# Kernel optimization log

Hardware: AMD Instinct MI355X
Metric: run time of the kernel (lower is better)

The kernel has to match this reference:

```python
import jax, jax.numpy as jnp
import numpy as np
from jax import lax

# Static problem sizes (see shape_source)
B, C, N = 32, 512, 64
SENTS_PER_VIDEO = 4
TARGETS_PER_SENT = 2
S = B * SENTS_PER_VIDEO          # 128 sentences
M = S * TARGETS_PER_SENT         # 256 target moments
P = N * (N + 1) // 2             # 2080 valid proposals (upper-tri mask2d)
T_TEMP = 0.1
MARGIN = 0.0
NEG_IOU = 0.5
K_TOP = 1                        # pos_topk
WEIGHT = 1.0


def setup_inputs() -> dict:
    key = jax.random.key(0)
    k1, k2, k3, k4 = jax.random.split(key, 4)
    return {
        "video_feats": jax.random.normal(k1, (B, C, N, N), jnp.float32),
        "sents_feats": jax.random.normal(k2, (S, C), jnp.float32),
        "num_sentences": jnp.full((B,), SENTS_PER_VIDEO, jnp.int32),
        "num_targets": jnp.full((S,), TARGETS_PER_SENT, jnp.int32),
        "iou2d": jax.random.uniform(k3, (S, N, N), jnp.float32),
        "iou2ds": jax.random.uniform(k4, (M, N, N), jnp.float32),
        "mask2d": jnp.triu(jnp.ones((N, N), bool)),
        "epoch": 0,  # < start_DNS_epoch -> DNS branch skipped
    }


def _log_cross_entropy(pos_scores, all_scores, neg_mask, t, m):
    # Faithful to LogCrossEntropy.forward
    pos_exp = jnp.exp((pos_scores - m) / t)
    neg_exp_sum = jnp.sum(jnp.exp(all_scores / t) * neg_mask, axis=-1)
    loss = -((pos_scores - m) / t - jnp.log(pos_exp + neg_exp_sum))
    return jnp.mean(loss)


def _l2_normalize(x, axis=-1, eps=1e-12):
    n = jnp.linalg.norm(x, axis=axis, keepdims=True)
    return x / jnp.maximum(n, eps)


def reference(video_feats, sents_feats, num_sentences, num_targets,
              iou2d, iou2ds, mask2d, epoch):
    # Compact valid proposals (P is static: upper-triangular mask2d)
    idx = jnp.nonzero(mask2d.reshape(-1), size=P)[0]              # (P,)
    v = video_feats.reshape(B, C, N * N)[:, :, idx]               # (B,C,P)
    v = jnp.transpose(v, (0, 2, 1))                               # (B,P,C)
    iou2d_f = iou2d.reshape(S, N * N)[:, idx]                     # (S,P)
    iou2ds_f = iou2ds.reshape(M, N * N)[:, idx]                   # (M,P)

    v = _l2_normalize(v)
    sents = _l2_normalize(sents_feats)

    scatter_s2v = jnp.repeat(jnp.arange(B), num_sentences, total_repeat_length=S)
    scatter_m2s = jnp.repeat(jnp.arange(S), num_targets, total_repeat_length=M)
    scatter_m2v = scatter_s2v[scatter_m2s]

    # top-K proposals per target moment by IoU
    topk_idx = lax.top_k(iou2ds_f, K_TOP)[1]                      # (M,K)
    topk_v = jnp.take_along_axis(v[scatter_m2v], topk_idx[:, :, None], axis=1)  # (M,K,C)

    # inter-video loss
    inter_video_pos = jnp.einsum('mkc,mc->mk', topk_v, sents[scatter_m2s])  # (M,K)
    inter_video_all = jnp.einsum('mkc,sc->mks', topk_v, sents)              # (M,K,S)
    inter_video_neg_mask = (~jnp.eye(S, dtype=bool))[scatter_m2s][:, None, :]  # (M,1,S)
    loss_inter_video = _log_cross_entropy(
        inter_video_pos, inter_video_all, inter_video_neg_mask, T_TEMP, MARGIN)

    # inter-query loss
    inter_query_pos = inter_video_pos                              # (M,K)
    inter_query_all = (sents @ v.reshape(B * P, C).T)[:, None, :]  # (S,1,B*P)
    # pos_mask: block-diagonal per video, refined by IoU > neg_iou inside own block
    onehot = jnp.eye(B, dtype=bool)[scatter_s2v]                   # (S,B)
    pos_mask = (onehot[:, :, None] & (iou2d_f > NEG_IOU)[:, None, :]).reshape(S, B * P)
    inter_query_neg_mask = (~pos_mask)[:, None, :]                 # (S,1,B*P)
    loss_inter_query = _log_cross_entropy(
        inter_query_pos, inter_query_all[scatter_m2s],
        inter_query_neg_mask[scatter_m2s], T_TEMP, MARGIN)

    total = (loss_inter_video + loss_inter_query) * WEIGHT
    return total, loss_inter_video, loss_inter_query
```

## Files before the change

### kernel.cpp

```cpp
#include <hip/hip_runtime.h>
#include <cstdint>

#define BB 32
#define CC 512
#define NSQ 4096
#define SS 128
#define MM 256
#define PP 2080
#define JJ (BB*PP)

#define WS_SN     0
#define WS_SNB    262144
#define WS_IDX    393216
#define WS_IV     401536
#define WS_NEGQ   532608

typedef short bf16x8 __attribute__((ext_vector_type(8)));
typedef float f32x4  __attribute__((ext_vector_type(4)));

__device__ __forceinline__ unsigned short f2bf(float x) {
    unsigned int u = __float_as_uint(x);
    unsigned int r = (u + 0x7fffu + ((u >> 16) & 1u)) >> 16;
    return (unsigned short)r;
}

__global__ void k_prep(const float* __restrict__ sents, float* __restrict__ sn,
                       unsigned short* __restrict__ snb,
                       int* __restrict__ idx, float* __restrict__ negq) {
    const int blk = blockIdx.x, t = threadIdx.x;
    if (blk < 128) {
        __shared__ float red[256];
        const float* row = sents + (size_t)blk * CC;
        float x0 = row[t], x1 = row[t + 256];
        red[t] = x0 * x0 + x1 * x1;
        __syncthreads();
        for (int off = 128; off > 0; off >>= 1) {
            if (t < off) red[t] += red[t + off];
            __syncthreads();
        }
        float rn = 1.0f / fmaxf(sqrtf(red[0]), 1e-12f);
        float y0 = x0 * rn, y1 = x1 * rn;
        sn[(size_t)blk * CC + t]        = y0;
        sn[(size_t)blk * CC + t + 256]  = y1;
        snb[(size_t)blk * CC + t]       = f2bf(y0);
        snb[(size_t)blk * CC + t + 256] = f2bf(y1);
    } else if (blk < 144) {
        int i = (blk - 128) * 256 + t;
        int r = i >> 6, c = i & 63;
        if (c >= r) {
            int p = r * 64 - (r * (r - 1)) / 2 + (c - r);
            idx[p] = i;
        }
    } else {
        if (t < 128) negq[t] = 0.0f;
    }
}

__global__ void k_fused(const float* __restrict__ video, const float* __restrict__ sn,
                        const float* __restrict__ iou2ds, const int* __restrict__ idx,
                        float* __restrict__ iv) {
    const int m = blockIdx.x, t = threadIdx.x;
    __shared__ float sv[256];
    __shared__ int   si[256];
    __shared__ float tvs[512];
    __shared__ float red[256];

    {
        float best = -1e30f; int bi = 1 << 30;
        const float* row = iou2ds + (size_t)m * NSQ;
        for (int p = t; p < PP; p += 256) {
            float v = row[idx[p]];
            if (v > best || (v == best && p < bi)) { best = v; bi = p; }
        }
        sv[t] = best; si[t] = bi;
        __syncthreads();
        for (int off = 128; off > 0; off >>= 1) {
            if (t < off) {
                float v2 = sv[t + off]; int i2 = si[t + off];
                if (v2 > sv[t] || (v2 == sv[t] && i2 < si[t])) { sv[t] = v2; si[t] = i2; }
            }
            __syncthreads();
        }
    }
    const int flat = idx[si[0]];
    const int b = m >> 3;

    const float* base = video + (size_t)b * CC * NSQ + flat;
    float x0 = base[(size_t)t * NSQ];
    float x1 = base[(size_t)(t + 256) * NSQ];
    red[t] = x0 * x0 + x1 * x1;
    __syncthreads();
    for (int off = 128; off > 0; off >>= 1) {
        if (t < off) red[t] += red[t + off];
        __syncthreads();
    }
    float rn = 1.0f / fmaxf(sqrtf(red[0]), 1e-12f);
    tvs[t] = x0 * rn;
    tvs[t + 256] = x1 * rn;
    __syncthreads();

    const int s = t & 127, h = t >> 7;
    const float4* a4 = (const float4*)(tvs + h * 256);
    const float4* b4 = (const float4*)(sn + (size_t)s * CC + h * 256);
    float acc = 0.f;
#pragma unroll 8
    for (int c = 0; c < 64; c++) {
        float4 a = a4[c], bb = b4[c];
        acc += a.x * bb.x + a.y * bb.y + a.z * bb.z + a.w * bb.w;
    }
    __syncthreads();
    red[t] = acc;
    __syncthreads();
    if (t < 128) iv[(size_t)m * SS + t] = red[t] + red[t + 128];
}

#define BK 64
#define LDK 72

__global__ __launch_bounds__(256)
void k_big(const float* __restrict__ video, const unsigned short* __restrict__ snb,
           const float* __restrict__ iou2d, const int* __restrict__ idx,
           float* __restrict__ negq) {
    __shared__ unsigned short sA[128 * LDK];
    __shared__ unsigned short vB[128 * LDK];
    __shared__ int   colb[128], colflat[128];
    __shared__ float colrn[128];
    __shared__ float sqpart[256];
    __shared__ float red[128][17];

    const int t    = threadIdx.x;
    const int w    = t >> 6;
    const int lane = t & 63;
    const int q    = lane >> 4;
    const int l15  = lane & 15;
    const int j0   = blockIdx.x * 128;

    if (t < 128) {
        int col = j0 + t;
        int b = col / PP;
        colb[t] = b;
        colflat[t] = idx[col - b * PP];
    }

    const int jj = t & 127;
    const int kh = t >> 7;
    int colL = j0 + jj;
    int bL = colL / PP;
    int flatL = idx[colL - bL * PP];
    const float* vbase = video + (size_t)bL * (CC * NSQ) + flatL;

    f32x4 acc[2][8];
#pragma unroll
    for (int i = 0; i < 2; i++)
#pragma unroll
        for (int j = 0; j < 8; j++) acc[i][j] = (f32x4){0.f, 0.f, 0.f, 0.f};

    float sqa = 0.f;

    for (int k0 = 0; k0 < CC; k0 += BK) {
        __syncthreads();
#pragma unroll
        for (int it = 0; it < 4; it++) {
            int lin = t + it * 256;
            int row = lin >> 3, kc = (lin & 7) * 8;
            bf16x8 v = *(const bf16x8*)(snb + (size_t)row * CC + k0 + kc);
            *(bf16x8*)(sA + row * LDK + kc) = v;
        }
        {
            const float* vp = vbase + (size_t)(k0 + kh * 32) * NSQ;
#pragma unroll
            for (int g = 0; g < 4; g++) {
                unsigned short buf[8];
#pragma unroll
                for (int i = 0; i < 8; i++) {
                    float x = vp[(size_t)(g * 8 + i) * NSQ];
                    sqa += x * x;
                    buf[i] = f2bf(x);
                }
                *(bf16x8*)(vB + jj * LDK + kh * 32 + g * 8) = *(bf16x8*)buf;
            }
        }
        __syncthreads();
#pragma unroll
        for (int ks = 0; ks < BK; ks += 32) {
            bf16x8 a[2], bfr[8];
#pragma unroll
            for (int rt = 0; rt < 2; rt++) {
                int row = w * 32 + rt * 16 + l15;
                a[rt] = *(const bf16x8*)(sA + row * LDK + ks + q * 8);
            }
#pragma unroll
            for (int ct = 0; ct < 8; ct++) {
                int col = ct * 16 + l15;
                bfr[ct] = *(const bf16x8*)(vB + col * LDK + ks + q * 8);
            }
#pragma unroll
            for (int rt = 0; rt < 2; rt++)
#pragma unroll
                for (int ct = 0; ct < 8; ct++)
                    acc[rt][ct] = __builtin_amdgcn_mfma_f32_16x16x32_bf16(
                        a[rt], bfr[ct], acc[rt][ct], 0, 0, 0);
        }
    }

    sqpart[t] = sqa;
    __syncthreads();
    if (t < 128) colrn[t] = 1.0f / fmaxf(sqrtf(sqpart[t] + sqpart[t + 128]), 1e-12f);
    __syncthreads();

#pragma unroll
    for (int rt = 0; rt < 2; rt++) {
#pragma unroll
        for (int r = 0; r < 4; r++) {
            int s = w * 32 + rt * 16 + q * 4 + r;
            float rowsum = 0.f;
#pragma unroll
            for (int ct = 0; ct < 8; ct++) {
                int c = ct * 16 + l15;
                float sc = acc[rt][ct][r] * colrn[c];
                float e = expf(sc * 10.0f);
                if ((s >> 2) == colb[c]) {
                    if (iou2d[(size_t)s * NSQ + colflat[c]] > 0.5f) e = 0.f;
                }
                rowsum += e;
            }
            red[s][l15] = rowsum;
        }
    }
    __syncthreads();
    if (t < 128) {
        float tot = 0.f;
#pragma unroll
        for (int x = 0; x < 16; x++) tot += red[t][x];
        atomicAdd(&negq[t], tot);
    }
}

__global__ void k_final(const float* __restrict__ iv, const float* __restrict__ negq,
                        float* __restrict__ out) {
    const int t = threadIdx.x;
    __shared__ float rv[256], rq[256];
    const float* row = iv + (size_t)t * SS;
    const int ms = t >> 1;
    float pos = row[ms];
    float nv = 0.f;
    for (int s = 0; s < SS; s++) {
        float e = expf(row[s] * 10.0f);
        if (s == ms) e = 0.f;
        nv += e;
    }
    float pe = expf(pos * 10.0f);
    float lv = logf(pe + nv) - pos * 10.0f;
    float lq = logf(pe + negq[ms]) - pos * 10.0f;
    rv[t] = lv; rq[t] = lq;
    __syncthreads();
    for (int off = 128; off > 0; off >>= 1) {
        if (t < off) { rv[t] += rv[t + off]; rq[t] += rq[t + off]; }
        __syncthreads();
    }
    if (t == 0) {
        float liv = rv[0] / 256.f, liq = rq[0] / 256.f;
        out[0] = liv + liq;
        out[1] = liv;
        out[2] = liq;
    }
}

extern "C" void kernel_launch(void* const* d_in, const int* in_sizes, int n_in,
                              void* d_out, int out_size, void* d_ws, size_t ws_size,
                              hipStream_t stream) {
    const float* video  = (const float*)d_in[0];
    const float* sents  = (const float*)d_in[1];
    const float* iou2d  = (const float*)d_in[4];
    const float* iou2ds = (const float*)d_in[5];
    float* out = (float*)d_out;

    char* ws = (char*)d_ws;
    float*          sn   = (float*)(ws + WS_SN);
    unsigned short* snb  = (unsigned short*)(ws + WS_SNB);
    int*            idx  = (int*)(ws + WS_IDX);
    float*          iv   = (float*)(ws + WS_IV);
    float*          negq = (float*)(ws + WS_NEGQ);

    k_prep <<<145, 256, 0, stream>>>(sents, sn, snb, idx, negq);
    k_big  <<<JJ / 128, 256, 0, stream>>>(video, snb, iou2d, idx, negq);
    k_fused<<<MM,  256, 0, stream>>>(video, sn, iou2ds, idx, iv);
    k_final<<<1,   256, 0, stream>>>(iv, negq, out);
}
```

Baseline: 438.2 us.

## Fuse all stages into one persistent cooperative kernel with atomic job queue

Replaces the four separate launches with a single cooperative persistent kernel of 512 blocks. The blocks run the prep stage, sync across the grid, then pull GEMM tiles and top-1 moment jobs from an atomic counter, sync across the grid again, and block 0 computes the final loss. The GEMM path also register-prefetches the next K-slab of video features to overlap global loads with MFMA work. This removes launch gaps and tail effects at the cost of grid syncs, extra register pressure from the 32-float prefetch buffer, and a residency requirement for the cooperative launch, with the old kernels kept as a fallback.

```diff
diff --git a/kernel.cpp b/kernel.cpp
--- a/kernel.cpp
+++ b/kernel.cpp
@@ -1,5 +1,8 @@
 #include <hip/hip_runtime.h>
+#include <hip/hip_cooperative_groups.h>
 #include <cstdint>
+
+namespace cg = cooperative_groups;
 
 #define BB 32
 #define CC 512
@@ -8,12 +11,15 @@
 #define MM 256
 #define PP 2080
 #define JJ (BB*PP)
+#define NTILE (JJ/128)
+#define NJOBS (NTILE + MM)
 
 #define WS_SN     0
 #define WS_SNB    262144
 #define WS_IDX    393216
 #define WS_IV     401536
 #define WS_NEGQ   532608
+#define WS_CTR    533120
 
 typedef short bf16x8 __attribute__((ext_vector_type(8)));
 typedef float f32x4  __attribute__((ext_vector_type(4)));
@@ -22,6 +28,275 @@
     unsigned int u = __float_as_uint(x);
     unsigned int r = (u + 0x7fffu + ((u >> 16) & 1u)) >> 16;
     return (unsigned short)r;
+}
+
+#define BK 64
+#define LDK 72
+
+struct SMemG {
+    unsigned short sA[128 * LDK];
+    unsigned short vB[128 * LDK];
+    int   colb[128];
+    int   colflat[128];
+    float colrn[128];
+    float sqpart[256];
+    float red[128][17];
+};
+struct SMemM {
+    float sv[256];
+    int   si[256];
+    float tvs[512];
+    float red[256];
+};
+struct SMemP {
+    float red[256];
+};
+union SMem { SMemG g; SMemM m; SMemP p; };
+
+__global__ __launch_bounds__(256, 2)
+void k_all(const float* __restrict__ video, const float* __restrict__ sents,
+           const float* __restrict__ iou2d, const float* __restrict__ iou2ds,
+           float* __restrict__ sn, unsigned short* __restrict__ snb,
+           int* __restrict__ idx, float* __restrict__ iv,
+           float* __restrict__ negq, int* __restrict__ ctr,
+           float* __restrict__ out)
+{
+    __shared__ SMem sm;
+    __shared__ int jobS;
+    const int t   = threadIdx.x;
+    const int blk = blockIdx.x;
+    cg::grid_group grid = cg::this_grid();
+
+    if (blk < 128) {
+        const float* row = sents + (size_t)blk * CC;
+        float x0 = row[t], x1 = row[t + 256];
+        sm.p.red[t] = x0 * x0 + x1 * x1;
+        __syncthreads();
+        for (int off = 128; off > 0; off >>= 1) {
+            if (t < off) sm.p.red[t] += sm.p.red[t + off];
+            __syncthreads();
+        }
+        float rn = 1.0f / fmaxf(sqrtf(sm.p.red[0]), 1e-12f);
+        float y0 = x0 * rn, y1 = x1 * rn;
+        sn[(size_t)blk * CC + t]        = y0;
+        sn[(size_t)blk * CC + t + 256]  = y1;
+        snb[(size_t)blk * CC + t]       = f2bf(y0);
+        snb[(size_t)blk * CC + t + 256] = f2bf(y1);
+    } else if (blk < 144) {
+        int i = (blk - 128) * 256 + t;
+        int r = i >> 6, c = i & 63;
+        if (c >= r) {
+            int p = r * 64 - (r * (r - 1)) / 2 + (c - r);
+            idx[p] = i;
+        }
+    } else if (blk == 144) {
+        if (t < 128) negq[t] = 0.0f;
+        if (t == 128) *ctr = 0;
+    }
+    grid.sync();
+
+    const int w    = t >> 6;
+    const int lane = t & 63;
+    const int q    = lane >> 4;
+    const int l15  = lane & 15;
+
+    for (;;) {
+        __syncthreads();
+        if (t == 0) jobS = atomicAdd(ctr, 1);
+        __syncthreads();
+        const int job = jobS;
+        if (job >= NJOBS) break;
+
+        if (job < NTILE) {
+            const int j0 = job * 128;
+            if (t < 128) {
+                int col = j0 + t;
+                int b = col / PP;
+                sm.g.colb[t] = b;
+                sm.g.colflat[t] = idx[col - b * PP];
+            }
+            const int jj = t & 127;
+            const int kh = t >> 7;
+            int colL = j0 + jj;
+            int bL = colL / PP;
+            int flatL = idx[colL - bL * PP];
+            const float* vbase = video + (size_t)bL * (CC * NSQ) + flatL;
+
+            f32x4 acc[2][8];
+#pragma unroll
+            for (int i = 0; i < 2; i++)
+#pragma unroll
+                for (int j = 0; j < 8; j++) acc[i][j] = (f32x4){0.f, 0.f, 0.f, 0.f};
+            float sqa = 0.f;
+
+            float pre[32];
+            {
+                const float* vp = vbase + (size_t)(kh * 32) * NSQ;
+#pragma unroll
+                for (int i = 0; i < 32; i++) pre[i] = vp[(size_t)i * NSQ];
+            }
+
+            for (int k0 = 0; k0 < CC; k0 += BK) {
+                __syncthreads();
+#pragma unroll
+                for (int it = 0; it < 4; it++) {
+                    int lin = t + it * 256;
+                    int row = lin >> 3, kc = (lin & 7) * 8;
+                    bf16x8 v = *(const bf16x8*)(snb + (size_t)row * CC + k0 + kc);
+                    *(bf16x8*)(sm.g.sA + row * LDK + kc) = v;
+                }
+#pragma unroll
+                for (int g = 0; g < 4; g++) {
+                    unsigned short buf[8];
+#pragma unroll
+                    for (int i = 0; i < 8; i++) {
+                        float x = pre[g * 8 + i];
+                        sqa += x * x;
+                        buf[i] = f2bf(x);
+                    }
+                    *(bf16x8*)(sm.g.vB + jj * LDK + kh * 32 + g * 8) = *(bf16x8*)buf;
+                }
+                __syncthreads();
+                if (k0 + BK < CC) {
+                    const float* vp = vbase + (size_t)(k0 + BK + kh * 32) * NSQ;
+#pragma unroll
+                    for (int i = 0; i < 32; i++) pre[i] = vp[(size_t)i * NSQ];
+                }
+#pragma unroll
+                for (int ks = 0; ks < BK; ks += 32) {
+                    bf16x8 a[2], bfr[8];
+#pragma unroll
+                    for (int rt = 0; rt < 2; rt++) {
+                        int row = w * 32 + rt * 16 + l15;
+                        a[rt] = *(const bf16x8*)(sm.g.sA + row * LDK + ks + q * 8);
+                    }
+#pragma unroll
+                    for (int ct = 0; ct < 8; ct++) {
+                        int col = ct * 16 + l15;
+                        bfr[ct] = *(const bf16x8*)(sm.g.vB + col * LDK + ks + q * 8);
+                    }
+#pragma unroll
+                    for (int rt = 0; rt < 2; rt++)
+#pragma unroll
+                        for (int ct = 0; ct < 8; ct++)
+                            acc[rt][ct] = __builtin_amdgcn_mfma_f32_16x16x32_bf16(
+                                a[rt], bfr[ct], acc[rt][ct], 0, 0, 0);
+                }
+            }
+
+            sm.g.sqpart[t] = sqa;
+            __syncthreads();
+            if (t < 128)
+                sm.g.colrn[t] = 1.0f / fmaxf(sqrtf(sm.g.sqpart[t] + sm.g.sqpart[t + 128]), 1e-12f);
+            __syncthreads();
+
+#pragma unroll
+            for (int rt = 0; rt < 2; rt++) {
+#pragma unroll
+                for (int r = 0; r < 4; r++) {
+                    int s = w * 32 + rt * 16 + q * 4 + r;
+                    float rowsum = 0.f;
+#pragma unroll
+                    for (int ct = 0; ct < 8; ct++) {
+                        int c = ct * 16 + l15;
+                        float sc = acc[rt][ct][r] * sm.g.colrn[c];
+                        float e = expf(sc * 10.0f);
+                        if ((s >> 2) == sm.g.colb[c]) {
+                            if (iou2d[(size_t)s * NSQ + sm.g.colflat[c]] > 0.5f) e = 0.f;
+                        }
+                        rowsum += e;
+                    }
+                    sm.g.red[s][l15] = rowsum;
+                }
+            }
+            __syncthreads();
+            if (t < 128) {
+                float tot = 0.f;
+#pragma unroll
+                for (int x = 0; x < 16; x++) tot += sm.g.red[t][x];
+                atomicAdd(&negq[t], tot);
+            }
+        } else {
+            const int m = job - NTILE;
+            {
+                float best = -1e30f; int bi = 1 << 30;
+                const float* row = iou2ds + (size_t)m * NSQ;
+                for (int p = t; p < PP; p += 256) {
+                    float v = row[idx[p]];
+                    if (v > best || (v == best && p < bi)) { best = v; bi = p; }
+                }
+                sm.m.sv[t] = best; sm.m.si[t] = bi;
+                __syncthreads();
+                for (int off = 128; off > 0; off >>= 1) {
+                    if (t < off) {
+                        float v2 = sm.m.sv[t + off]; int i2 = sm.m.si[t + off];
+                        if (v2 > sm.m.sv[t] || (v2 == sm.m.sv[t] && i2 < sm.m.si[t])) {
+                            sm.m.sv[t] = v2; sm.m.si[t] = i2;
+                        }
+                    }
+                    __syncthreads();
+                }
+            }
+            const int flat = idx[sm.m.si[0]];
+            const int b = m >> 3;
+
+            const float* base = video + (size_t)b * CC * NSQ + flat;
+            float x0 = base[(size_t)t * NSQ];
+            float x1 = base[(size_t)(t + 256) * NSQ];
+            sm.m.red[t] = x0 * x0 + x1 * x1;
+            __syncthreads();
+            for (int off = 128; off > 0; off >>= 1) {
+                if (t < off) sm.m.red[t] += sm.m.red[t + off];
+                __syncthreads();
+            }
+            float rn = 1.0f / fmaxf(sqrtf(sm.m.red[0]), 1e-12f);
+            sm.m.tvs[t] = x0 * rn;
+            sm.m.tvs[t + 256] = x1 * rn;
+            __syncthreads();
+
+            const int s = t & 127, h = t >> 7;
+            const float4* a4 = (const float4*)(sm.m.tvs + h * 256);
+            const float4* b4 = (const float4*)(sn + (size_t)s * CC + h * 256);
+            float acc2 = 0.f;
+#pragma unroll 8
+            for (int c = 0; c < 64; c++) {
+                float4 a = a4[c], bb = b4[c];
+                acc2 += a.x * bb.x + a.y * bb.y + a.z * bb.z + a.w * bb.w;
+            }
+            __syncthreads();
+            sm.m.red[t] = acc2;
+            __syncthreads();
+            if (t < 128) iv[(size_t)m * SS + t] = sm.m.red[t] + sm.m.red[t + 128];
+        }
+    }
+    grid.sync();
+
+    if (blk == 0) {
+        const float* row = iv + (size_t)t * SS;
+        const int ms = t >> 1;
+        float pos = row[ms];
+        float nv = 0.f;
+        for (int s2 = 0; s2 < SS; s2++) {
+            float e = expf(row[s2] * 10.0f);
+            if (s2 == ms) e = 0.f;
+            nv += e;
+        }
+        float pe = expf(pos * 10.0f);
+        float lv = logf(pe + nv) - pos * 10.0f;
+        float lq = logf(pe + negq[ms]) - pos * 10.0f;
+        sm.m.sv[t] = lv; sm.m.red[t] = lq;
+        __syncthreads();
+        for (int off = 128; off > 0; off >>= 1) {
+            if (t < off) { sm.m.sv[t] += sm.m.sv[t + off]; sm.m.red[t] += sm.m.red[t + off]; }
+            __syncthreads();
+        }
+        if (t == 0) {
+            float liv = sm.m.sv[0] / 256.f, liq = sm.m.red[0] / 256.f;
+            out[0] = liv + liq;
+            out[1] = liv;
+            out[2] = liq;
+        }
+    }
 }
 
 __global__ void k_prep(const float* __restrict__ sents, float* __restrict__ sn,
@@ -64,7 +339,6 @@
     __shared__ int   si[256];
     __shared__ float tvs[512];
     __shared__ float red[256];
-
     {
         float best = -1e30f; int bi = 1 << 30;
         const float* row = iou2ds + (size_t)m * NSQ;
@@ -84,7 +358,6 @@
     }
     const int flat = idx[si[0]];
     const int b = m >> 3;
-
     const float* base = video + (size_t)b * CC * NSQ + flat;
     float x0 = base[(size_t)t * NSQ];
     float x1 = base[(size_t)(t + 256) * NSQ];
@@ -98,7 +371,6 @@
     tvs[t] = x0 * rn;
     tvs[t + 256] = x1 * rn;
     __syncthreads();
-
     const int s = t & 127, h = t >> 7;
     const float4* a4 = (const float4*)(tvs + h * 256);
     const float4* b4 = (const float4*)(sn + (size_t)s * CC + h * 256);
@@ -113,9 +385,6 @@
     __syncthreads();
     if (t < 128) iv[(size_t)m * SS + t] = red[t] + red[t + 128];
 }
-
-#define BK 64
-#define LDK 72
 
 __global__ __launch_bounds__(256)
 void k_big(const float* __restrict__ video, const unsigned short* __restrict__ snb,
@@ -141,7 +410,6 @@
         colb[t] = b;
         colflat[t] = idx[col - b * PP];
     }
-
     const int jj = t & 127;
     const int kh = t >> 7;
     int colL = j0 + jj;
@@ -154,7 +422,6 @@
     for (int i = 0; i < 2; i++)
 #pragma unroll
         for (int j = 0; j < 8; j++) acc[i][j] = (f32x4){0.f, 0.f, 0.f, 0.f};
-
     float sqa = 0.f;
 
     for (int k0 = 0; k0 < CC; k0 += BK) {
@@ -281,9 +548,17 @@
     int*            idx  = (int*)(ws + WS_IDX);
     float*          iv   = (float*)(ws + WS_IV);
     float*          negq = (float*)(ws + WS_NEGQ);
-
-    k_prep <<<145, 256, 0, stream>>>(sents, sn, snb, idx, negq);
-    k_big  <<<JJ / 128, 256, 0, stream>>>(video, snb, iou2d, idx, negq);
-    k_fused<<<MM,  256, 0, stream>>>(video, sn, iou2ds, idx, iv);
-    k_final<<<1,   256, 0, stream>>>(iv, negq, out);
-}
+    int*            ctr  = (int*)(ws + WS_CTR);
+
+    void* args[] = { (void*)&video, (void*)&sents, (void*)&iou2d, (void*)&iou2ds,
+                     (void*)&sn, (void*)&snb, (void*)&idx, (void*)&iv,
+                     (void*)&negq, (void*)&ctr, (void*)&out };
+    hipError_t err = hipLaunchCooperativeKernel((const void*)k_all, dim3(512), dim3(256),
+                                                args, 0, stream);
+    if (err != hipSuccess) {
+        k_prep <<<145, 256, 0, stream>>>(sents, sn, snb, idx, negq);
+        k_big  <<<JJ / 128, 256, 0, stream>>>(video, snb, iou2d, idx, negq);
+        k_fused<<<MM,  256, 0, stream>>>(video, sn, iou2ds, idx, iv);
+        k_final<<<1,   256, 0, stream>>>(iv, negq, out);
+    }
+}
```

Result: slower. 539.4 us (+23.1%).

## Compute dense N×N score tile per video with coalesced float4 loads, masking invalid proposals

Applied to the files above, without the earlier changes.

Replaces the gathered-column GEMM over compacted upper-triangular proposals with a dense GEMM over all N*N positions per video. Columns map directly to flat indices, so the video tensor is read with contiguous float4 loads instead of scattered per-column gathers, and lower-triangle entries are masked out in the epilogue. This removes the index indirection and uncoalesced global reads, at the cost of about twice the MFMA work and exp evaluations on positions that are then discarded. Column norms are now reduced through a shared-memory partial-sum table.

```diff
diff --git a/kernel.cpp b/kernel.cpp
--- a/kernel.cpp
+++ b/kernel.cpp
@@ -7,7 +7,6 @@
 #define SS 128
 #define MM 256
 #define PP 2080
-#define JJ (BB*PP)
 
 #define WS_SN     0
 #define WS_SNB    262144
@@ -56,6 +55,141 @@
     }
 }
 
+#define BK 64
+#define LDK 72
+
+__global__ __launch_bounds__(256)
+void k_bigd(const float* __restrict__ video, const unsigned short* __restrict__ snb,
+            const float* __restrict__ iou2d, float* __restrict__ negq) {
+    __shared__ char smem[36864];
+    unsigned short* sA = (unsigned short*)smem;
+    unsigned short* vB = (unsigned short*)(smem + 18432);
+
+    const int t    = threadIdx.x;
+    const int w    = t >> 6;
+    const int lane = t & 63;
+    const int q    = lane >> 4;
+    const int l15  = lane & 15;
+
+    const int b  = blockIdx.x >> 5;
+    const int j0 = (blockIdx.x & 31) * 128;
+
+    const int cg = t & 31;
+    const int kr = t >> 5;
+
+    f32x4 acc[2][8];
+#pragma unroll
+    for (int i = 0; i < 2; i++)
+#pragma unroll
+        for (int j = 0; j < 8; j++) acc[i][j] = (f32x4){0.f, 0.f, 0.f, 0.f};
+    float sq0 = 0.f, sq1 = 0.f, sq2 = 0.f, sq3 = 0.f;
+
+    for (int k0 = 0; k0 < CC; k0 += BK) {
+        __syncthreads();
+#pragma unroll
+        for (int it = 0; it < 4; it++) {
+            int lin = t + it * 256;
+            int row = lin >> 3, kc = (lin & 7) * 8;
+            bf16x8 v = *(const bf16x8*)(snb + (size_t)row * CC + k0 + kc);
+            *(bf16x8*)(sA + row * LDK + kc) = v;
+        }
+        float4 r0[4], r1[4];
+#pragma unroll
+        for (int i = 0; i < 4; i++) {
+            int k = 2 * (kr + 8 * i);
+            const float* p = video + ((size_t)b * CC + k0 + k) * NSQ + j0 + 4 * cg;
+            r0[i] = *(const float4*)p;
+            r1[i] = *(const float4*)(p + NSQ);
+        }
+#pragma unroll
+        for (int i = 0; i < 4; i++) {
+            int kp = kr + 8 * i;
+            sq0 += r0[i].x * r0[i].x + r1[i].x * r1[i].x;
+            sq1 += r0[i].y * r0[i].y + r1[i].y * r1[i].y;
+            sq2 += r0[i].z * r0[i].z + r1[i].z * r1[i].z;
+            sq3 += r0[i].w * r0[i].w + r1[i].w * r1[i].w;
+            unsigned int p0 = (unsigned int)f2bf(r0[i].x) | ((unsigned int)f2bf(r1[i].x) << 16);
+            unsigned int p1 = (unsigned int)f2bf(r0[i].y) | ((unsigned int)f2bf(r1[i].y) << 16);
+            unsigned int p2 = (unsigned int)f2bf(r0[i].z) | ((unsigned int)f2bf(r1[i].z) << 16);
+            unsigned int p3 = (unsigned int)f2bf(r0[i].w) | ((unsigned int)f2bf(r1[i].w) << 16);
+            *(unsigned int*)(vB + (4 * cg + 0) * LDK + 2 * kp) = p0;
+            *(unsigned int*)(vB + (4 * cg + 1) * LDK + 2 * kp) = p1;
+            *(unsigned int*)(vB + (4 * cg + 2) * LDK + 2 * kp) = p2;
+            *(unsigned int*)(vB + (4 * cg + 3) * LDK + 2 * kp) = p3;
+        }
+        __syncthreads();
+#pragma unroll
+        for (int ks = 0; ks < BK; ks += 32) {
+            bf16x8 a[2], bfr[8];
+#pragma unroll
+            for (int rt = 0; rt < 2; rt++) {
+                int row = w * 32 + rt * 16 + l15;
+                a[rt] = *(const bf16x8*)(sA + row * LDK + ks + q * 8);
+            }
+#pragma unroll
+            for (int ct = 0; ct < 8; ct++) {
+                int col = ct * 16 + l15;
+                bfr[ct] = *(const bf16x8*)(vB + col * LDK + ks + q * 8);
+            }
+#pragma unroll
+            for (int rt = 0; rt < 2; rt++)
+#pragma unroll
+                for (int ct = 0; ct < 8; ct++)
+                    acc[rt][ct] = __builtin_amdgcn_mfma_f32_16x16x32_bf16(
+                        a[rt], bfr[ct], acc[rt][ct], 0, 0, 0);
+        }
+    }
+    __syncthreads();
+
+    float* sqred = (float*)smem;
+    float* redp  = (float*)(smem + 4608);
+    float* colrn = (float*)(smem + 13312);
+
+    sqred[(4 * cg + 0) * 9 + kr] = sq0;
+    sqred[(4 * cg + 1) * 9 + kr] = sq1;
+    sqred[(4 * cg + 2) * 9 + kr] = sq2;
+    sqred[(4 * cg + 3) * 9 + kr] = sq3;
+    __syncthreads();
+    if (t < 128) {
+        float ssum = 0.f;
+#pragma unroll
+        for (int x = 0; x < 8; x++) ssum += sqred[t * 9 + x];
+        colrn[t] = 1.0f / fmaxf(sqrtf(ssum), 1e-12f);
+    }
+    __syncthreads();
+
+#pragma unroll
+    for (int rt = 0; rt < 2; rt++) {
+#pragma unroll
+        for (int r = 0; r < 4; r++) {
+            int s = w * 32 + rt * 16 + q * 4 + r;
+            bool myvid = ((s >> 2) == b);
+            float rowsum = 0.f;
+#pragma unroll
+            for (int ct = 0; ct < 8; ct++) {
+                int c = ct * 16 + l15;
+                int j = j0 + c;
+                bool valid = (j & 63) >= (j >> 6);
+                float e = 0.f;
+                if (valid) {
+                    float sc = acc[rt][ct][r] * colrn[c];
+                    e = expf(sc * 10.0f);
+                    if (myvid && iou2d[(size_t)s * NSQ + j] > 0.5f) e = 0.f;
+                }
+                rowsum += e;
+            }
+            redp[s * 17 + l15] = rowsum;
+        }
+    }
+    __syncthreads();
+    if (t < 128) {
+        float tot = 0.f;
+#pragma unroll
+        for (int x = 0; x < 16; x++) tot += redp[t * 17 + x];
+        atomicAdd(&negq[t], tot);
+    }
+}
+
 __global__ void k_fused(const float* __restrict__ video, const float* __restrict__ sn,
                         const float* __restrict__ iou2ds, const int* __restrict__ idx,
                         float* __restrict__ iv) {
@@ -112,128 +246,6 @@
     red[t] = acc;
     __syncthreads();
     if (t < 128) iv[(size_t)m * SS + t] = red[t] + red[t + 128];
-}
-
-#define BK 64
-#define LDK 72
-
-__global__ __launch_bounds__(256)
-void k_big(const float* __restrict__ video, const unsigned short* __restrict__ snb,
-           const float* __restrict__ iou2d, const int* __restrict__ idx,
-           float* __restrict__ negq) {
-    __shared__ unsigned short sA[128 * LDK];
-    __shared__ unsigned short vB[128 * LDK];
-    __shared__ int   colb[128], colflat[128];
-    __shared__ float colrn[128];
-    __shared__ float sqpart[256];
-    __shared__ float red[128][17];
-
-    const int t    = threadIdx.x;
-    const int w    = t >> 6;
-    const int lane = t & 63;
-    const int q    = lane >> 4;
-    const int l15  = lane & 15;
-    const int j0   = blockIdx.x * 128;
-
-    if (t < 128) {
-        int col = j0 + t;
-        int b = col / PP;
-        colb[t] = b;
-        colflat[t] = idx[col - b * PP];
-    }
-
-    const int jj = t & 127;
-    const int kh = t >> 7;
-    int colL = j0 + jj;
-    int bL = colL / PP;
-    int flatL = idx[colL - bL * PP];
-    const float* vbase = video + (size_t)bL * (CC * NSQ) + flatL;
-
-    f32x4 acc[2][8];
-#pragma unroll
-    for (int i = 0; i < 2; i++)
-#pragma unroll
-        for (int j = 0; j < 8; j++) acc[i][j] = (f32x4){0.f, 0.f, 0.f, 0.f};
-
-    float sqa = 0.f;
-
-    for (int k0 = 0; k0 < CC; k0 += BK) {
-        __syncthreads();
-#pragma unroll
-        for (int it = 0; it < 4; it++) {
-            int lin = t + it * 256;
-            int row = lin >> 3, kc = (lin & 7) * 8;
-            bf16x8 v = *(const bf16x8*)(snb + (size_t)row * CC + k0 + kc);
-            *(bf16x8*)(sA + row * LDK + kc) = v;
-        }
-        {
-            const float* vp = vbase + (size_t)(k0 + kh * 32) * NSQ;
-#pragma unroll
-            for (int g = 0; g < 4; g++) {
-                unsigned short buf[8];
-#pragma unroll
-                for (int i = 0; i < 8; i++) {
-                    float x = vp[(size_t)(g * 8 + i) * NSQ];
-                    sqa += x * x;
-                    buf[i] = f2bf(x);
-                }
-                *(bf16x8*)(vB + jj * LDK + kh * 32 + g * 8) = *(bf16x8*)buf;
-            }
-        }
-        __syncthreads();
-#pragma unroll
-        for (int ks = 0; ks < BK; ks += 32) {
-            bf16x8 a[2], bfr[8];
-#pragma unroll
-            for (int rt = 0; rt < 2; rt++) {
-                int row = w * 32 + rt * 16 + l15;
-                a[rt] = *(const bf16x8*)(sA + row * LDK + ks + q * 8);
-            }
-#pragma unroll
-            for (int ct = 0; ct < 8; ct++) {
-                int col = ct * 16 + l15;
-                bfr[ct] = *(const bf16x8*)(vB + col * LDK + ks + q * 8);
-            }
-#pragma unroll
-            for (int rt = 0; rt < 2; rt++)
-#pragma unroll
-                for (int ct = 0; ct < 8; ct++)
-                    acc[rt][ct] = __builtin_amdgcn_mfma_f32_16x16x32_bf16(
-                        a[rt], bfr[ct], acc[rt][ct], 0, 0, 0);
-        }
-    }
-
-    sqpart[t] = sqa;
-    __syncthreads();
-    if (t < 128) colrn[t] = 1.0f / fmaxf(sqrtf(sqpart[t] + sqpart[t + 128]), 1e-12f);
-    __syncthreads();
-
-#pragma unroll
-    for (int rt = 0; rt < 2; rt++) {
-#pragma unroll
-        for (int r = 0; r < 4; r++) {
-            int s = w * 32 + rt * 16 + q * 4 + r;
-            float rowsum = 0.f;
-#pragma unroll
-            for (int ct = 0; ct < 8; ct++) {
-                int c = ct * 16 + l15;
-                float sc = acc[rt][ct][r] * colrn[c];
-                float e = expf(sc * 10.0f);
-                if ((s >> 2) == colb[c]) {
-                    if (iou2d[(size_t)s * NSQ + colflat[c]] > 0.5f) e = 0.f;
-                }
-                rowsum += e;
-            }
-            red[s][l15] = rowsum;
-        }
-    }
-    __syncthreads();
-    if (t < 128) {
-        float tot = 0.f;
-#pragma unroll
-        for (int x = 0; x < 16; x++) tot += red[t][x];
-        atomicAdd(&negq[t], tot);
-    }
 }
 
 __global__ void k_final(const float* __restrict__ iv, const float* __restrict__ negq,
@@ -283,7 +295,7 @@
     float*          negq = (float*)(ws + WS_NEGQ);
 
     k_prep <<<145, 256, 0, stream>>>(sents, sn, snb, idx, negq);
-    k_big  <<<JJ / 128, 256, 0, stream>>>(video, snb, iou2d, idx, negq);
-    k_fused<<<MM,  256, 0, stream>>>(video, sn, iou2ds, idx, iv);
-    k_final<<<1,   256, 0, stream>>>(iv, negq, out);
-}
+    k_bigd <<<BB * 32, 256, 0, stream>>>(video, snb, iou2d, negq);
+    k_fused<<<MM, 256, 0, stream>>>(video, sn, iou2ds, idx, iv);
+    k_final<<<1, 256, 0, stream>>>(iv, negq, out);
+}
```

Measured after the change: 421.0 us. -3.9%, faster.
